# Optimization experiments

Hardware: AMD Instinct MI355X
Metric: run time of the kernel (lower is better)

Reference implementation:

```python
import jax, jax.numpy as jnp
import numpy as np

B, T, D_IN, D_OUT = 4, 2048, 1024, 1024


def setup_inputs() -> dict:
    key = jax.random.key(0)
    k0, k1, k2, k3 = jax.random.split(key, 4)
    token_embed = jax.random.normal(k0, (B, T, D_IN), dtype=jnp.float32)
    # torch Linear weight is [out, in]; store transposed [in, out] for x @ W
    Wq = jax.random.normal(k1, (D_IN, D_OUT), dtype=jnp.float32) * (1.0 / np.sqrt(D_IN))
    Wk = jax.random.normal(k2, (D_IN, D_OUT), dtype=jnp.float32) * (1.0 / np.sqrt(D_IN))
    Wv = jax.random.normal(k3, (D_IN, D_OUT), dtype=jnp.float32) * (1.0 / np.sqrt(D_IN))
    return {"token_embed": token_embed, "Wq": Wq, "Wk": Wk, "Wv": Wv}


def reference(token_embed, Wq, Wk, Wv):
    # token_embed: [B, T, d_in]
    num_token = token_embed.shape[1]
    q = jnp.einsum("btd,de->bte", token_embed, Wq)  # [B, T, d_out]
    k = jnp.einsum("btd,de->bte", token_embed, Wk)
    v = jnp.einsum("btd,de->bte", token_embed, Wv)
    scores = jnp.einsum("bqe,bke->bqk", q, k)  # [B, T, T]
    # causal mask: strictly-upper-triangular positions set to -inf
    causal = jnp.triu(jnp.ones((num_token, num_token), dtype=bool), k=1)
    scores = jnp.where(causal[None, :, :], -jnp.inf, scores)
    # NOTE: faithful to source bug: scale by sqrt(seq_len) (keys.shape[1]), not sqrt(d_out)
    scale = jnp.asarray(num_token, dtype=scores.dtype) ** 0.5
    attn = jax.nn.softmax(scores / scale, axis=-1)
    # dropout prob is 0 -> identity
    context = jnp.einsum("bqk,bke->bqe", attn, v)  # [B, T, d_out]
    return context
```

## Files before the change

### kernel.cpp

```cpp
#include <hip/hip_runtime.h>
#include <cstdint>
#include <cstddef>
#include <math.h>


typedef __attribute__((ext_vector_type(4))) float f32x4;
typedef __attribute__((ext_vector_type(8))) short s16x8;

#define AS1(p) ((const __attribute__((address_space(1))) void*)(p))
#define AS3(p) ((__attribute__((address_space(3))) void*)(p))
#define BARRIER() asm volatile("s_barrier" ::: "memory")
#define W4 asm volatile("s_waitcnt vmcnt(4)" ::: "memory")
#define W3 asm volatile("s_waitcnt vmcnt(3)" ::: "memory")
#define W0c asm volatile("s_waitcnt vmcnt(0)" ::: "memory")
#define LGKM(n) do { asm volatile("s_waitcnt lgkmcnt(" #n ")" ::: "memory"); \
                     __builtin_amdgcn_sched_barrier(0); } while (0)
#define WNONE ((void)0)
#define NOISSUE ((void)0)

static __device__ __forceinline__ unsigned short f2bf(float x) {
  unsigned int u = __float_as_uint(x);
  unsigned int r = u + 0x7FFFu + ((u >> 16) & 1u);
  return (unsigned short)(r >> 16);
}
static __device__ __forceinline__ float bf2f(unsigned short h) {
  return __uint_as_float(((unsigned int)h) << 16);
}

__global__ __launch_bounds__(256) void k_cvt(const float* __restrict__ X,
                                             const float* __restrict__ W0p,
                                             const float* __restrict__ W1p,
                                             const float* __restrict__ W2p,
                                             unsigned short* __restrict__ Xb,
                                             unsigned short* __restrict__ Wt) {
  __shared__ float tile[64][65];
  const int bx = blockIdx.x;
  if (bx < 4096) {
    size_t i = ((size_t)bx * 256 + threadIdx.x) * 8;
    float4 a = *(const float4*)(X + i);
    float4 b = *(const float4*)(X + i + 4);
    union { unsigned short us[8]; uint4 v; } o;
    o.us[0] = f2bf(a.x); o.us[1] = f2bf(a.y); o.us[2] = f2bf(a.z); o.us[3] = f2bf(a.w);
    o.us[4] = f2bf(b.x); o.us[5] = f2bf(b.y); o.us[6] = f2bf(b.z); o.us[7] = f2bf(b.w);
    *(uint4*)(Xb + i) = o.v;
    return;
  }
  const int bx2 = bx - 4096;
  const int z = bx2 >> 8, t = bx2 & 255;
  const float* W = z == 0 ? W0p : (z == 1 ? W1p : W2p);
  unsigned short* dst = Wt + (size_t)z * 1048576;
  const int k0 = (t >> 4) * 64, n0 = (t & 15) * 64;
  const int tr = threadIdx.x >> 4, tc = (threadIdx.x & 15) * 4;
  for (int i = 0; i < 4; ++i) {
    int r = tr + i * 16;
    float4 v = *(const float4*)(W + (size_t)(k0 + r) * 1024 + n0 + tc);
    tile[r][tc + 0] = v.x; tile[r][tc + 1] = v.y;
    tile[r][tc + 2] = v.z; tile[r][tc + 3] = v.w;
  }
  __syncthreads();
  for (int i = 0; i < 4; ++i) {
    int r = tr + i * 16;
    ushort4 o;
    o.x = f2bf(tile[tc + 0][r]); o.y = f2bf(tile[tc + 1][r]);
    o.z = f2bf(tile[tc + 2][r]); o.w = f2bf(tile[tc + 3][r]);
    *(ushort4*)(dst + (size_t)(n0 + r) * 1024 + k0 + tc) = o;
  }
}

static __device__ __forceinline__ void stage2(const char* src, size_t ld128, char* dst) {
  __builtin_amdgcn_global_load_lds(AS1(src), AS3(dst), 16, 0, 0);
  __builtin_amdgcn_global_load_lds(AS1(src + ld128), AS3(dst + 8192), 16, 0, 0);
}

template <class FA, class FB>
static __device__ __forceinline__ void core256(const char* __restrict__ As,
                                               const char* __restrict__ Bs,
                                               size_t ldA128, size_t ldB128,
                                               FA offA, FB offB,
                                               int nkt, char* smem, f32x4 (&acc)[8][4]) {
  const int tid = threadIdx.x, w = tid >> 6, lane = tid & 63;
  const int lr = lane & 15, lq = lane >> 4;
  const int wm = (w >> 2) * 128, wn = (w & 3) * 64;
  char* ldsA = smem + w * 1024;
  char* ldsB = smem + 65536 + w * 1024;
  s16x8 afA[4], afB[4], bfr[4];

#define STG_A(t, h) stage2(As + offA((t), (h)), ldA128, ldsA + (((t) & 1) * 2 + (h)) * 16384)
#define STG_B(t, h) stage2(Bs + offB((t), (h)), ldB128, ldsB + (((t) & 1) * 2 + (h)) * 16384)
#define STG(t, h) do { STG_A(t, h); STG_B(t, h); } while (0)
#define RD_A(buf, h, r) (*(const s16x8*)(smem + ((buf) * 2 + (h)) * 16384 + (r) * 64 + ((lq ^ (((r) >> 1) & 3)) << 4)))
#define RD_B(buf, h, r) (*(const s16x8*)(smem + 65536 + ((buf) * 2 + (h)) * 16384 + (r) * 64 + ((lq ^ (((r) >> 1) & 3)) << 4)))
#define MMQ(AF, BF, base) \
  _Pragma("unroll") for (int i = 0; i < 4; ++i) \
  _Pragma("unroll") for (int c = 0; c < 4; ++c) \
    acc[(base) + i][c] = __builtin_amdgcn_mfma_f32_16x16x32_bf16(AF[i], BF[c], acc[(base) + i][c], 0, 0, 0)
#define PHASE(TT, HH, ISSUE, WVM) { \
    const int _bf = (TT) & 1; \
    _Pragma("unroll") for (int i = 0; i < 4; ++i) afA[i] = RD_A(_bf, HH, wm + i * 16 + lr); \
    _Pragma("unroll") for (int c = 0; c < 4; ++c) bfr[c] = RD_B(_bf, HH, wn + c * 16 + lr); \
    _Pragma("unroll") for (int i = 0; i < 4; ++i) afB[i] = RD_A(_bf, HH, wm + 64 + i * 16 + lr); \
    ISSUE; WVM; BARRIER(); \
    LGKM(4); \
    __builtin_amdgcn_s_setprio(1); \
    MMQ(afA, bfr, 0); \
    LGKM(0); \
    MMQ(afB, bfr, 4); \
    __builtin_amdgcn_s_setprio(0); \
  }

  STG(0, 0); STG(0, 1);
  W4; BARRIER();

  int t = 0;
  for (; t + 1 < nkt; ++t) {
    PHASE(t, 0, STG(t + 1, 0), W4)
    PHASE(t, 1, STG(t + 1, 1), W4)
  }
  PHASE(t, 0, NOISSUE, W0c)
  PHASE(t, 1, NOISSUE, WNONE)

#undef STG_A
#undef STG_B
#undef STG
#undef RD_A
#undef RD_B
#undef MMQ
#undef PHASE
}

template <class FA, class FB>
static __device__ __forceinline__ void core_v(const char* __restrict__ As,
                                              const char* __restrict__ Bs,
                                              size_t ldA128, size_t ldB128,
                                              FA offA, FB offB,
                                              int nkt, char* smem, f32x4 (&acc)[4][4]) {
  const int tid = threadIdx.x, w = tid >> 6, lane = tid & 63;
  const int lr = lane & 15, lq = lane >> 4;
  const int wm = (w >> 2) * 64, wn = (w & 3) * 64;
  char* ldsA = smem + w * 1024;
  char* ldsB = smem + 32768 + w * 1024;
  s16x8 af[4], bfr[4];

#define STG_A(t, h) __builtin_amdgcn_global_load_lds(AS1(As + offA((t), (h))), \
    AS3(ldsA + (((t) & 1) * 2 + (h)) * 8192), 16, 0, 0)
#define STG_B(t, h) stage2(Bs + offB((t), (h)), ldB128, ldsB + (((t) & 1) * 2 + (h)) * 16384)
#define STG(t, h) do { STG_A(t, h); STG_B(t, h); } while (0)
#define RD_A(buf, h, r) (*(const s16x8*)(smem + ((buf) * 2 + (h)) * 8192 + (r) * 64 + ((lq ^ (((r) >> 1) & 3)) << 4)))
#define RD_B(buf, h, r) (*(const s16x8*)(smem + 32768 + ((buf) * 2 + (h)) * 16384 + (r) * 64 + ((lq ^ (((r) >> 1) & 3)) << 4)))
#define PHASE(TT, HH, ISSUE, WVM) { \
    const int _bf = (TT) & 1; \
    _Pragma("unroll") for (int i = 0; i < 4; ++i) af[i] = RD_A(_bf, HH, wm + i * 16 + lr); \
    _Pragma("unroll") for (int c = 0; c < 4; ++c) bfr[c] = RD_B(_bf, HH, wn + c * 16 + lr); \
    ISSUE; WVM; BARRIER(); \
    LGKM(0); \
    __builtin_amdgcn_s_setprio(1); \
    _Pragma("unroll") for (int i = 0; i < 4; ++i) \
    _Pragma("unroll") for (int c = 0; c < 4; ++c) \
      acc[i][c] = __builtin_amdgcn_mfma_f32_16x16x32_bf16(af[i], bfr[c], acc[i][c], 0, 0, 0); \
    __builtin_amdgcn_s_setprio(0); \
  }

  STG(0, 0); STG(0, 1);
  W3; BARRIER();

  int t = 0;
  for (; t + 1 < nkt; ++t) {
    PHASE(t, 0, STG(t + 1, 0), W3)
    PHASE(t, 1, STG(t + 1, 1), W3)
  }
  PHASE(t, 0, NOISSUE, W0c)
  PHASE(t, 1, NOISSUE, WNONE)

#undef STG_A
#undef STG_B
#undef STG
#undef RD_A
#undef RD_B
#undef PHASE
}

struct OffLinear {
  __device__ __forceinline__ size_t operator()(int t, int h) const {
    return (size_t)t * 128 + (size_t)h * 64;
  }
};
struct OffTriK {
  int k0;
  __device__ __forceinline__ size_t operator()(int t, int h) const {
    int g = k0 + t;
    return (size_t)(g >> 2) * 131072 + (size_t)(g & 3) * 128 + (size_t)h * 64;
  }
};
struct OffLinK {
  int k0;
  __device__ __forceinline__ size_t operator()(int t, int h) const {
    return (size_t)(k0 + t) * 128 + (size_t)h * 64;
  }
};

static __device__ __forceinline__ void lane_src(int& rowl, int& slot) {
  const int tid = threadIdx.x, w = tid >> 6, lane = tid & 63;
  rowl = w * 16 + (lane >> 2);
  slot = (lane & 3) ^ ((rowl >> 1) & 3);
}

__global__ __launch_bounds__(512, 2) void k_qk(const unsigned short* __restrict__ Xb,
                                               const unsigned short* __restrict__ Wt,
                                               unsigned short* __restrict__ Qm,
                                               unsigned short* __restrict__ Km) {
  __shared__ char smem[131072];
  const int by = blockIdx.y, z = by >> 2, q = by & 3, bx = blockIdx.x;
  const int m0 = bx * 256, n0 = q * 256;
  const char* A = (const char*)(Xb + (size_t)m0 * 1024);
  const char* B = (const char*)(Wt + (size_t)z * 1048576 + (size_t)n0 * 1024);
  int rowl, slot; lane_src(rowl, slot);
  const size_t lo = (size_t)rowl * 2048 + slot * 16;
  f32x4 acc[8][4];
#pragma unroll
  for (int i = 0; i < 8; ++i)
#pragma unroll
    for (int c = 0; c < 4; ++c) acc[i][c] = (f32x4){0.f, 0.f, 0.f, 0.f};
  core256(A + lo, B + lo, (size_t)128 * 2048, (size_t)128 * 2048,
          OffLinear{}, OffLinear{}, 16, smem, acc);
  unsigned short* C = z == 0 ? Qm : Km;
  const int tid = threadIdx.x, w = tid >> 6, lane = tid & 63;
  const int lr = lane & 15, lq = lane >> 4;
  const int wm = (w >> 2) * 128, wn = (w & 3) * 64;
#pragma unroll
  for (int fr = 0; fr < 8; ++fr)
#pragma unroll
    for (int fc = 0; fc < 4; ++fc)
#pragma unroll
      for (int i = 0; i < 4; ++i) {
        int row = m0 + wm + fr * 16 + lq * 4 + i;
        int col = n0 + wn + fc * 16 + lr;
        C[(size_t)row * 1024 + col] = f2bf(acc[fr][fc][i]);
      }
}

__global__ __launch_bounds__(512, 2) void k_v(const unsigned short* __restrict__ Xb,
                                              const unsigned short* __restrict__ Wt,
                                              unsigned short* __restrict__ Vt) {
  __shared__ char smem[98304];
  const int x = blockIdx.x;
  const int m0 = (x & 7) * 128, n0 = (x >> 3) * 256;
  const char* A = (const char*)(Wt + (size_t)2 * 1048576 + (size_t)m0 * 1024);
  const char* B = (const char*)(Xb + (size_t)n0 * 1024);
  int rowl, slot; lane_src(rowl, slot);
  const size_t lo = (size_t)rowl * 2048 + slot * 16;
  f32x4 acc[4][4];
#pragma unroll
  for (int a = 0; a < 4; ++a)
#pragma unroll
    for (int c = 0; c < 4; ++c) acc[a][c] = (f32x4){0.f, 0.f, 0.f, 0.f};
  core_v(A + lo, B + lo, (size_t)128 * 2048, (size_t)128 * 2048,
         OffLinear{}, OffLinear{}, 16, smem, acc);
  const int tid = threadIdx.x, w = tid >> 6, lane = tid & 63;
  const int lr = lane & 15, lq = lane >> 4;
  const int wm = (w >> 2) * 64, wn = (w & 3) * 64;
#pragma unroll
  for (int fr = 0; fr < 4; ++fr)
#pragma unroll
    for (int fc = 0; fc < 4; ++fc)
#pragma unroll
      for (int i = 0; i < 4; ++i) {
        int row = m0 + wm + fr * 16 + lq * 4 + i;
        int col = n0 + wn + fc * 16 + lr;
        Vt[((size_t)(col >> 11) * 1024 + row) * 2048 + (col & 2047)] = f2bf(acc[fr][fc][i]);
      }
}

__global__ __launch_bounds__(512, 2) void k_sg(const unsigned short* __restrict__ Qm,
                                               const unsigned short* __restrict__ Km,
                                               unsigned short* __restrict__ S) {
  __shared__ char smem[131072];
  const int id = blockIdx.x;
  int i = 0;
  while ((i + 1) * (i + 2) / 2 <= id) ++i;
  const int j = id - i * (i + 1) / 2;
  const int b = blockIdx.y;
  const int m0 = i * 256, n0 = j * 256;
  int rowl, slot; lane_src(rowl, slot);
  const size_t lo = (size_t)rowl * 2048 + slot * 16;
  f32x4 acc[8][4];
#pragma unroll
  for (int a = 0; a < 8; ++a)
#pragma unroll
    for (int c = 0; c < 4; ++c) acc[a][c] = (f32x4){0.f, 0.f, 0.f, 0.f};
  core256((const char*)(Qm + ((size_t)b * 2048 + m0) * 1024) + lo,
          (const char*)(Km + ((size_t)b * 2048 + n0) * 1024) + lo,
          (size_t)128 * 2048, (size_t)128 * 2048, OffLinear{}, OffLinear{}, 16, smem, acc);
  const float SCALE = 0.022097086912079608f;
  const int tid = threadIdx.x, w = tid >> 6, lane = tid & 63;
  const int lr = lane & 15, lq = lane >> 4;
  const int wm = (w >> 2) * 128, wn = (w & 3) * 64;
  unsigned short* tb = S + (((size_t)(b * 36 + id)) << 16);
#pragma unroll
  for (int fr = 0; fr < 8; ++fr)
#pragma unroll
    for (int fc = 0; fc < 4; ++fc)
#pragma unroll
      for (int i2 = 0; i2 < 4; ++i2) {
        int rl = wm + fr * 16 + lq * 4 + i2;
        int cl = wn + fc * 16 + lr;
        tb[(size_t)rl * 256 + cl] = f2bf(acc[fr][fc][i2] * SCALE);
      }
}

__global__ __launch_bounds__(256) void k_softmax(unsigned short* __restrict__ S) {
  const int tid = threadIdx.x, w = tid >> 6, lane = tid & 63;
  const int row = blockIdx.x * 4 + w;
  const int b = row >> 11, q = row & 2047;
  const int i = q >> 8, ntl = i + 1, rowL = q & 255;
  unsigned short* base = S + (((size_t)(b * 36 + (i * (i + 1)) / 2)) << 16)
                           + (size_t)rowL * 256 + lane * 4;
  float v[8][4];
#pragma unroll
  for (int t = 0; t < 8; ++t) {
    if (t < ntl) {
      ushort4 x = *(const ushort4*)(base + (size_t)t * 65536);
      int c0 = t * 256 + lane * 4;
      v[t][0] = (c0 + 0 <= q) ? bf2f(x.x) : -INFINITY;
      v[t][1] = (c0 + 1 <= q) ? bf2f(x.y) : -INFINITY;
      v[t][2] = (c0 + 2 <= q) ? bf2f(x.z) : -INFINITY;
      v[t][3] = (c0 + 3 <= q) ? bf2f(x.w) : -INFINITY;
    } else {
      v[t][0] = v[t][1] = v[t][2] = v[t][3] = -INFINITY;
    }
  }
  float m = -INFINITY;
#pragma unroll
  for (int t = 0; t < 8; ++t)
#pragma unroll
    for (int jj = 0; jj < 4; ++jj) m = fmaxf(m, v[t][jj]);
  for (int off = 32; off; off >>= 1) m = fmaxf(m, __shfl_xor(m, off));
  float s = 0.f;
#pragma unroll
  for (int t = 0; t < 8; ++t)
#pragma unroll
    for (int jj = 0; jj < 4; ++jj) { v[t][jj] = __expf(v[t][jj] - m); s += v[t][jj]; }
  for (int off = 32; off; off >>= 1) s += __shfl_xor(s, off);
  const float inv = 1.f / s;
#pragma unroll
  for (int t = 0; t < 8; ++t)
    if (t < ntl) {
      ushort4 o;
      o.x = f2bf(v[t][0] * inv); o.y = f2bf(v[t][1] * inv);
      o.z = f2bf(v[t][2] * inv); o.w = f2bf(v[t][3] * inv);
      *(ushort4*)(base + (size_t)t * 65536) = o;
    }
}

__device__ const int pvi[15] = {2, 5, 5, 7, 7, 4, 4, 6, 6, 1, 3, 3, 6, 7, 0};
__device__ const int pvk[15] = {0, 0, 12, 0, 12, 0, 10, 0, 10, 0, 0, 8, 20, 24, 0};
__device__ const int pvn[15] = {12, 12, 12, 12, 12, 10, 10, 10, 10, 8, 8, 8, 8, 8, 4};
__device__ const int pvp[15] = {-1, -1, 2, -1, 5, -1, 1, -1, 3, -1, -1, 0, 4, 6, -1};

__global__ __launch_bounds__(512, 2) void k_pv(const unsigned short* __restrict__ P,
                                               const unsigned short* __restrict__ Vt,
                                               float* __restrict__ out,
                                               float* __restrict__ part) {
  __shared__ char smem[131072];
  const int cx = blockIdx.x % 15;
  const int panel = blockIdx.x / 15;
  const int nt = panel & 3, b = panel >> 2;
  const int i = pvi[cx], k0 = pvk[cx], nkt = pvn[cx], psl = pvp[cx];
  const char* Pb = (const char*)P + (((size_t)(b * 36 + (i * (i + 1)) / 2)) << 17);
  int rowl, slot; lane_src(rowl, slot);
  const char* Asrc = Pb + (size_t)rowl * 512 + slot * 16;
  const char* Bsrc = (const char*)Vt + ((size_t)(b * 1024 + nt * 256 + rowl)) * 4096 + slot * 16;
  f32x4 acc[8][4];
#pragma unroll
  for (int a = 0; a < 8; ++a)
#pragma unroll
    for (int c = 0; c < 4; ++c) acc[a][c] = (f32x4){0.f, 0.f, 0.f, 0.f};
  core256(Asrc, Bsrc, (size_t)128 * 512, (size_t)128 * 4096,
          OffTriK{k0}, OffLinK{k0}, nkt, smem, acc);
  const int tid = threadIdx.x, w = tid >> 6, lane = tid & 63;
  const int lr = lane & 15, lq = lane >> 4;
  const int wm = (w >> 2) * 128, wn = (w & 3) * 64;
  if (psl < 0) {
#pragma unroll
    for (int fr = 0; fr < 8; ++fr)
#pragma unroll
      for (int fc = 0; fc < 4; ++fc)
#pragma unroll
        for (int i2 = 0; i2 < 4; ++i2) {
          int orow = i * 256 + wm + fr * 16 + lq * 4 + i2;
          int col = nt * 256 + wn + fc * 16 + lr;
          out[((size_t)b * 2048 + orow) * 1024 + col] = acc[fr][fc][i2];
        }
  } else {
    float* pt = part + ((size_t)(panel * 7 + psl)) * 65536;
#pragma unroll
    for (int fr = 0; fr < 8; ++fr)
#pragma unroll
      for (int fc = 0; fc < 4; ++fc)
#pragma unroll
        for (int i2 = 0; i2 < 4; ++i2) {
          int rl = wm + fr * 16 + lq * 4 + i2;
          int cl = wn + fc * 16 + lr;
          pt[(size_t)rl * 256 + cl] = acc[fr][fc][i2];
        }
  }
}

__global__ __launch_bounds__(256) void k_fix(float* __restrict__ out,
                                             const float* __restrict__ part) {
  const size_t e = ((size_t)blockIdx.x * 256 + threadIdx.x) * 4;
  const int b = (int)(e / 1310720);
  const int rem = (int)(e % 1310720);
  const int row = 768 + (rem >> 10);
  const int col = rem & 1023;
  const int i = row >> 8;
  const int nt = col >> 8;
  const int base4[5] = {0, 1, 2, 3, 5};
  const int cnt4[5] = {1, 1, 1, 2, 2};
  const int sb = base4[i - 3], cnt = cnt4[i - 3];
  const float* pt = part + ((size_t)((b * 4 + nt) * 7 + sb)) * 65536
                         + (size_t)(row & 255) * 256 + (col & 255);
  float* op = out + ((size_t)b * 2048 + row) * 1024 + col;
  float4 o = *(const float4*)op;
  float4 p0 = *(const float4*)pt;
  o.x += p0.x; o.y += p0.y; o.z += p0.z; o.w += p0.w;
  if (cnt == 2) {
    float4 p1 = *(const float4*)(pt + 65536);
    o.x += p1.x; o.y += p1.y; o.z += p1.z; o.w += p1.w;
  }
  *(float4*)op = o;
}

extern "C" void kernel_launch(void* const* d_in, const int* in_sizes, int n_in,
                              void* d_out, int out_size, void* d_ws, size_t ws_size,
                              hipStream_t stream) {
  const float* X  = (const float*)d_in[0];
  const float* W0p = (const float*)d_in[1];
  const float* W1p = (const float*)d_in[2];
  const float* W2p = (const float*)d_in[3];
  float* out = (float*)d_out;
  char* ws = (char*)d_ws;
  unsigned short* Xb = (unsigned short*)ws;
  unsigned short* Wt = (unsigned short*)(ws + (size_t)16777216);
  unsigned short* Qm = (unsigned short*)(ws + (size_t)23068672);
  unsigned short* Km = (unsigned short*)(ws + (size_t)39845888);
  unsigned short* Vt = (unsigned short*)(ws + (size_t)56623104);
  unsigned short* Sb = (unsigned short*)ws;
  float* Pp = (float*)(ws + (size_t)23068672);
  (void)in_sizes; (void)n_in; (void)out_size; (void)ws_size;

  hipLaunchKernelGGL(k_cvt, dim3(4864), dim3(256), 0, stream, X, W0p, W1p, W2p, Xb, Wt);
  hipLaunchKernelGGL(k_qk, dim3(32, 8), dim3(512), 0, stream, Xb, Wt, Qm, Km);
  hipLaunchKernelGGL(k_v, dim3(256), dim3(512), 0, stream, Xb, Wt, Vt);
  hipLaunchKernelGGL(k_sg, dim3(36, 4), dim3(512), 0, stream, Qm, Km, Sb);
  hipLaunchKernelGGL(k_softmax, dim3(2048), dim3(256), 0, stream, Sb);
  hipLaunchKernelGGL(k_pv, dim3(240), dim3(512), 0, stream, Sb, Vt, out, Pp);
  hipLaunchKernelGGL(k_fix, dim3(5120), dim3(256), 0, stream, out, Pp);
}
```

Before: 160.9 us.

## Restructure GEMM main loops to one barrier per k-tile with full prefetch

Both GEMM core loops now issue the global-to-LDS staging for both halves of the next k-tile at once. They process both halves of the current tile and use a single vmcnt(0) wait plus one barrier per iteration, instead of one barrier and a partial vmcnt wait per half. The aim is to halve the barrier count and to overlap LDS fragment reads for the second half with the first half's MFMAs. The trade-off is coarser waits: vmcnt(0) at the end of each tile means the prefetch has less slack to hide global latency.

```diff
diff --git a/kernel.cpp b/kernel.cpp
--- a/kernel.cpp
+++ b/kernel.cpp
@@ -10,13 +10,9 @@
 #define AS1(p) ((const __attribute__((address_space(1))) void*)(p))
 #define AS3(p) ((__attribute__((address_space(3))) void*)(p))
 #define BARRIER() asm volatile("s_barrier" ::: "memory")
-#define W4 asm volatile("s_waitcnt vmcnt(4)" ::: "memory")
-#define W3 asm volatile("s_waitcnt vmcnt(3)" ::: "memory")
 #define W0c asm volatile("s_waitcnt vmcnt(0)" ::: "memory")
 #define LGKM(n) do { asm volatile("s_waitcnt lgkmcnt(" #n ")" ::: "memory"); \
                      __builtin_amdgcn_sched_barrier(0); } while (0)
-#define WNONE ((void)0)
-#define NOISSUE ((void)0)
 
 static __device__ __forceinline__ unsigned short f2bf(float x) {
   unsigned int u = __float_as_uint(x);
@@ -94,30 +90,43 @@
   _Pragma("unroll") for (int i = 0; i < 4; ++i) \
   _Pragma("unroll") for (int c = 0; c < 4; ++c) \
     acc[(base) + i][c] = __builtin_amdgcn_mfma_f32_16x16x32_bf16(AF[i], BF[c], acc[(base) + i][c], 0, 0, 0)
-#define PHASE(TT, HH, ISSUE, WVM) { \
-    const int _bf = (TT) & 1; \
-    _Pragma("unroll") for (int i = 0; i < 4; ++i) afA[i] = RD_A(_bf, HH, wm + i * 16 + lr); \
-    _Pragma("unroll") for (int c = 0; c < 4; ++c) bfr[c] = RD_B(_bf, HH, wn + c * 16 + lr); \
-    _Pragma("unroll") for (int i = 0; i < 4; ++i) afB[i] = RD_A(_bf, HH, wm + 64 + i * 16 + lr); \
-    ISSUE; WVM; BARRIER(); \
-    LGKM(4); \
-    __builtin_amdgcn_s_setprio(1); \
-    MMQ(afA, bfr, 0); \
-    LGKM(0); \
-    MMQ(afB, bfr, 4); \
-    __builtin_amdgcn_s_setprio(0); \
-  }
 
   STG(0, 0); STG(0, 1);
-  W4; BARRIER();
-
-  int t = 0;
-  for (; t + 1 < nkt; ++t) {
-    PHASE(t, 0, STG(t + 1, 0), W4)
-    PHASE(t, 1, STG(t + 1, 1), W4)
-  }
-  PHASE(t, 0, NOISSUE, W0c)
-  PHASE(t, 1, NOISSUE, WNONE)
+  W0c; BARRIER();
+
+  for (int t = 0; t < nkt; ++t) {
+    const int _bf = t & 1;
+    const bool more = (t + 1) < nkt;
+#pragma unroll
+    for (int i = 0; i < 4; ++i) afA[i] = RD_A(_bf, 0, wm + i * 16 + lr);
+#pragma unroll
+    for (int c = 0; c < 4; ++c) bfr[c] = RD_B(_bf, 0, wn + c * 16 + lr);
+#pragma unroll
+    for (int i = 0; i < 4; ++i) afB[i] = RD_A(_bf, 0, wm + 64 + i * 16 + lr);
+    if (more) { STG(t + 1, 0); STG(t + 1, 1); }
+    LGKM(4);
+    __builtin_amdgcn_s_setprio(1);
+    MMQ(afA, bfr, 0);
+    LGKM(0);
+    __builtin_amdgcn_s_setprio(0);
+#pragma unroll
+    for (int i = 0; i < 4; ++i) afA[i] = RD_A(_bf, 1, wm + i * 16 + lr);
+    __builtin_amdgcn_s_setprio(1);
+    MMQ(afB, bfr, 4);
+    __builtin_amdgcn_s_setprio(0);
+#pragma unroll
+    for (int c = 0; c < 4; ++c) bfr[c] = RD_B(_bf, 1, wn + c * 16 + lr);
+#pragma unroll
+    for (int i = 0; i < 4; ++i) afB[i] = RD_A(_bf, 1, wm + 64 + i * 16 + lr);
+    LGKM(4);
+    __builtin_amdgcn_s_setprio(1);
+    MMQ(afA, bfr, 0);
+    LGKM(0);
+    MMQ(afB, bfr, 4);
+    __builtin_amdgcn_s_setprio(0);
+    if (more) { W0c; }
+    BARRIER();
+  }
 
 #undef STG_A
 #undef STG_B
@@ -125,7 +134,6 @@
 #undef RD_A
 #undef RD_B
 #undef MMQ
-#undef PHASE
 }
 
 template <class FA, class FB>
@@ -147,36 +155,44 @@
 #define STG(t, h) do { STG_A(t, h); STG_B(t, h); } while (0)
 #define RD_A(buf, h, r) (*(const s16x8*)(smem + ((buf) * 2 + (h)) * 8192 + (r) * 64 + ((lq ^ (((r) >> 1) & 3)) << 4)))
 #define RD_B(buf, h, r) (*(const s16x8*)(smem + 32768 + ((buf) * 2 + (h)) * 16384 + (r) * 64 + ((lq ^ (((r) >> 1) & 3)) << 4)))
-#define PHASE(TT, HH, ISSUE, WVM) { \
-    const int _bf = (TT) & 1; \
-    _Pragma("unroll") for (int i = 0; i < 4; ++i) af[i] = RD_A(_bf, HH, wm + i * 16 + lr); \
-    _Pragma("unroll") for (int c = 0; c < 4; ++c) bfr[c] = RD_B(_bf, HH, wn + c * 16 + lr); \
-    ISSUE; WVM; BARRIER(); \
-    LGKM(0); \
-    __builtin_amdgcn_s_setprio(1); \
-    _Pragma("unroll") for (int i = 0; i < 4; ++i) \
-    _Pragma("unroll") for (int c = 0; c < 4; ++c) \
-      acc[i][c] = __builtin_amdgcn_mfma_f32_16x16x32_bf16(af[i], bfr[c], acc[i][c], 0, 0, 0); \
-    __builtin_amdgcn_s_setprio(0); \
-  }
+#define MMV(AF, BF) \
+  _Pragma("unroll") for (int i = 0; i < 4; ++i) \
+  _Pragma("unroll") for (int c = 0; c < 4; ++c) \
+    acc[i][c] = __builtin_amdgcn_mfma_f32_16x16x32_bf16(AF[i], BF[c], acc[i][c], 0, 0, 0)
 
   STG(0, 0); STG(0, 1);
-  W3; BARRIER();
-
-  int t = 0;
-  for (; t + 1 < nkt; ++t) {
-    PHASE(t, 0, STG(t + 1, 0), W3)
-    PHASE(t, 1, STG(t + 1, 1), W3)
-  }
-  PHASE(t, 0, NOISSUE, W0c)
-  PHASE(t, 1, NOISSUE, WNONE)
+  W0c; BARRIER();
+
+  for (int t = 0; t < nkt; ++t) {
+    const int _bf = t & 1;
+    const bool more = (t + 1) < nkt;
+#pragma unroll
+    for (int i = 0; i < 4; ++i) af[i] = RD_A(_bf, 0, wm + i * 16 + lr);
+#pragma unroll
+    for (int c = 0; c < 4; ++c) bfr[c] = RD_B(_bf, 0, wn + c * 16 + lr);
+    if (more) { STG(t + 1, 0); STG(t + 1, 1); }
+    LGKM(0);
+    __builtin_amdgcn_s_setprio(1);
+    MMV(af, bfr);
+    __builtin_amdgcn_s_setprio(0);
+#pragma unroll
+    for (int i = 0; i < 4; ++i) af[i] = RD_A(_bf, 1, wm + i * 16 + lr);
+#pragma unroll
+    for (int c = 0; c < 4; ++c) bfr[c] = RD_B(_bf, 1, wn + c * 16 + lr);
+    LGKM(0);
+    __builtin_amdgcn_s_setprio(1);
+    MMV(af, bfr);
+    __builtin_amdgcn_s_setprio(0);
+    if (more) { W0c; }
+    BARRIER();
+  }
 
 #undef STG_A
 #undef STG_B
 #undef STG
 #undef RD_A
 #undef RD_B
-#undef PHASE
+#undef MMV
 }
 
 struct OffLinear {
```

New measurement: 162.4 us. Within noise of the previous version (+0.9%).
